# Optimization experiments

Hardware: AMD Instinct MI355X
Metric: run time of the kernel (lower is better)

Reference implementation:

```python
import jax, jax.numpy as jnp
import numpy as np

B, N, C = 8, 4096, 512
NUM_HEADS = 8
HEAD_DIM = C // NUM_HEADS
POS_RES = 32  # only table with res <= max_resolution=32


def _interp_linear(pos, out_len):
    # F.interpolate(mode='linear', align_corners=False) along the length axis (axis 1)
    in_len = pos.shape[1]
    scale = in_len / out_len
    coords = (jnp.arange(out_len, dtype=jnp.float32) + 0.5) * scale - 0.5
    coords = jnp.clip(coords, 0.0, in_len - 1)
    i0 = jnp.floor(coords).astype(jnp.int32)
    i1 = jnp.minimum(i0 + 1, in_len - 1)
    w = (coords - i0.astype(jnp.float32))[None, :, None]
    return pos[:, i0, :] * (1.0 - w) + pos[:, i1, :] * w


def setup_inputs():
    key = jax.random.key(0)
    k = jax.random.split(key, 4)
    x = jax.random.normal(k[0], (B, N, C), jnp.float32)
    pos_32 = jax.random.normal(k[1], (1, POS_RES ** 3, C), jnp.float32)  # torch.randn init
    s = 1.0 / np.sqrt(C)
    w_qkv = jax.random.normal(k[2], (C, 3 * C), jnp.float32) * s
    b_qkv = jnp.zeros((3 * C,), jnp.float32)
    w_proj = jax.random.normal(k[3], (C, C), jnp.float32) * s
    b_proj = jnp.zeros((C,), jnp.float32)
    return {"x": x, "pos_32": pos_32, "w_qkv": w_qkv, "b_qkv": b_qkv,
            "w_proj": w_proj, "b_proj": b_proj, "resolution": 16}


def reference(x, pos_32, w_qkv, b_qkv, w_proj, b_proj, resolution):
    Bx, Nx, Cx = x.shape
    target_len = resolution ** 3  # 4096 -> nearest table pos_32 is interpolated down
    pos = pos_32 if pos_32.shape[1] == target_len else _interp_linear(pos_32, target_len)
    if pos.shape[1] == Nx:
        x = x + pos
    qkv = (x @ w_qkv + b_qkv).reshape(Bx, Nx, 3, NUM_HEADS, HEAD_DIM)
    q, k, v = qkv[:, :, 0], qkv[:, :, 1], qkv[:, :, 2]  # each [B, N, H, D]
    # Faithful to source: q,k,v are NOT permuted to [B,H,N,D], so q @ k.T
    # contracts head_dim per token, yielding [B, N, H, H] head-axis attention.
    attn = jnp.einsum('bnid,bnjd->bnij', q, k) / np.sqrt(HEAD_DIM)
    attn = jax.nn.softmax(attn, axis=-1)
    out = jnp.einsum('bnij,bnjd->bnid', attn, v)  # [B, N, H, D]
    # torch: .transpose(1, 2).reshape(B, N, C) -> flatten of [B, H, N, D]
    out = jnp.transpose(out, (0, 2, 1, 3)).reshape(Bx, Nx, Cx)
    return out @ w_proj + b_proj
```

## Files before the change

kernel.cpp:

```cpp
#include <hip/hip_runtime.h>
#include <hip/hip_bf16.h>

using bf16 = __hip_bfloat16;
typedef __attribute__((ext_vector_type(8))) short short8;
typedef __attribute__((ext_vector_type(4))) float f32x4;

#define AS1U(p) ((const __attribute__((address_space(1))) unsigned int*)(p))
#define AS3U(p) ((__attribute__((address_space(3))) unsigned int*)(p))

__device__ __forceinline__ float bflo(unsigned u) { return __uint_as_float(u << 16); }
__device__ __forceinline__ float bfhi(unsigned u) { return __uint_as_float(u & 0xffff0000u); }
__device__ __forceinline__ unsigned short f2bf(float f) {
    union { float f; unsigned u; } v{f};
    unsigned r = v.u + 0x7fffu + ((v.u >> 16) & 1u);
    return (unsigned short)(r >> 16);
}

__global__ __launch_bounds__(256) void kprep(const float* __restrict__ wq,
                                             const float* __restrict__ wp,
                                             const float* __restrict__ x,
                                             const float* __restrict__ pos,
                                             bf16* __restrict__ wqT,
                                             bf16* __restrict__ wpT,
                                             bf16* __restrict__ xp) {
    int bid = blockIdx.x;
    __shared__ float t[32][33];
    if (bid < 1024) {
        const float* in; bf16* out; int Cc, bx, by;
        if (bid < 768) { in = wq; out = wqT; Cc = 1536; bx = bid % 48; by = bid / 48; }
        else { int i = bid - 768; in = wp; out = wpT; Cc = 512; bx = i & 15; by = i >> 4; }
        const int R = 512;
        int tx = threadIdx.x & 31, ty = threadIdx.x >> 5;
        int c0 = bx * 32, r0 = by * 32;
#pragma unroll
        for (int i = 0; i < 4; ++i)
            t[ty + i * 8][tx] = in[(size_t)(r0 + ty + i * 8) * Cc + c0 + tx];
        __syncthreads();
#pragma unroll
        for (int i = 0; i < 4; ++i)
            out[(size_t)(c0 + ty + i * 8) * R + r0 + tx] = __float2bfloat16(t[tx][ty + i * 8]);
    } else {
        size_t idx4 = (size_t)(bid - 1024) * 256 + threadIdx.x;
        size_t e = idx4 * 4;
        int c = (int)(e & 511);
        size_t m = e >> 9;
        int n = (int)(m & 4095);
        float4 xv = *(const float4*)(x + e);
        float4 p3 = *(const float4*)(pos + (size_t)(n * 8 + 3) * 512 + c);
        float4 p4 = *(const float4*)(pos + (size_t)(n * 8 + 4) * 512 + c);
        unsigned r[2];
        float v0 = xv.x + 0.5f * (p3.x + p4.x);
        float v1 = xv.y + 0.5f * (p3.y + p4.y);
        float v2 = xv.z + 0.5f * (p3.z + p4.z);
        float v3 = xv.w + 0.5f * (p3.w + p4.w);
        r[0] = (unsigned)f2bf(v0) | ((unsigned)f2bf(v1) << 16);
        r[1] = (unsigned)f2bf(v2) | ((unsigned)f2bf(v3) << 16);
        *(uint2*)(xp + e) = *(uint2*)r;
    }
}

template <typename OutT>
__global__ __launch_bounds__(512, 2) void kgemm8(const bf16* __restrict__ A,
                                                 const bf16* __restrict__ Bt,
                                                 const float* __restrict__ bias,
                                                 OutT* __restrict__ C,
                                                 int M, int N, int K_) {
    constexpr int K = 512;
    __shared__ __align__(16) char smem[131072];
    const int tid = threadIdx.x;
    const int lane = tid & 63, wave = tid >> 6;
    const int wm = wave >> 2, wn = wave & 3;
    const int fr = lane & 15;
    const int g = lane >> 4;

    const int p_rd = (((fr & 1) << 2) | g) ^ ((fr >> 1) & 7);
    const int tbA = (wm * 64 + (fr >> 1)) * 128 + p_rd * 16;
    const int tbB = (wn * 32 + (fr >> 1)) * 128 + p_rd * 16;

    const int ntn = N >> 8;
    const int nwg = gridDim.x;
    const int bid = blockIdx.x;
    const int swz = (bid & 7) * (nwg >> 3) + (bid >> 3);
    const int bm = (swz / ntn) << 8;
    const int bn = (swz % ntn) << 8;

    const int q = (lane & 7) ^ (lane >> 3);
    const int srow = wave * 32 + 2 * (lane >> 3) + ((q >> 2) & 1);
    const int scol = (q & 3) * 8;
    const bf16* sA[2]; const bf16* sB[2];
#pragma unroll
    for (int g2 = 0; g2 < 2; ++g2) {
        sA[g2] = A  + (size_t)(bm + srow + g2 * 16) * K + scol;
        sB[g2] = Bt + (size_t)(bn + srow + g2 * 16) * K + scol;
    }
    const int dA0 = wave * 2048, dA1 = wave * 2048 + 1024;

    f32x4 acc[8][4];
#pragma unroll
    for (int i = 0; i < 8; ++i)
#pragma unroll
        for (int j = 0; j < 4; ++j) acc[i][j] = f32x4{0.f, 0.f, 0.f, 0.f};

    auto stageA = [&](int kt, int slot) {
        char* d = smem + slot * 32768;
        __builtin_amdgcn_global_load_lds(AS1U(sA[0] + kt * 32), AS3U(d + dA0), 16, 0, 0);
        __builtin_amdgcn_global_load_lds(AS1U(sA[1] + kt * 32), AS3U(d + dA1), 16, 0, 0);
    };
    auto stageB = [&](int kt, int slot) {
        char* d = smem + slot * 32768 + 16384;
        __builtin_amdgcn_global_load_lds(AS1U(sB[0] + kt * 32), AS3U(d + dA0), 16, 0, 0);
        __builtin_amdgcn_global_load_lds(AS1U(sB[1] + kt * 32), AS3U(d + dA1), 16, 0, 0);
    };

    stageA(0, 0); stageB(0, 0);
    stageA(1, 1); stageB(1, 1);
    stageA(2, 2); stageB(2, 2);
    asm volatile("s_waitcnt vmcnt(8)" ::: "memory");
    __builtin_amdgcn_s_barrier();

#pragma unroll
    for (int t = 0; t < 16; ++t) {
        const int rd = t & 3, wrs = (t + 3) & 3;
        const char* pa = smem + rd * 32768;
        const char* pb = pa + 16384;
        if (t < 13) { stageA(t + 3, wrs); stageB(t + 3, wrs); }
        short8 af[8], bfr[4];
#pragma unroll
        for (int mi = 0; mi < 8; ++mi) af[mi] = *(const short8*)(pa + tbA + mi * 1024);
#pragma unroll
        for (int nj = 0; nj < 4; ++nj) bfr[nj] = *(const short8*)(pb + tbB + nj * 1024);
#pragma unroll
        for (int mi = 0; mi < 8; ++mi)
#pragma unroll
            for (int nj = 0; nj < 4; ++nj)
                acc[mi][nj] = __builtin_amdgcn_mfma_f32_16x16x32_bf16(af[mi], bfr[nj], acc[mi][nj], 0, 0, 0);
        asm volatile("s_waitcnt lgkmcnt(0)" ::: "memory");
        if (t <= 12)      asm volatile("s_waitcnt vmcnt(8)" ::: "memory");
        else if (t == 13) asm volatile("s_waitcnt vmcnt(4)" ::: "memory");
        else if (t == 14) asm volatile("s_waitcnt vmcnt(0)" ::: "memory");
        __builtin_amdgcn_sched_barrier(0);
        __builtin_amdgcn_s_barrier();
    }

#pragma unroll
    for (int mi = 0; mi < 8; ++mi) {
#pragma unroll
        for (int nj = 0; nj < 4; ++nj) {
            int col = bn + wn * 64 + nj * 16 + fr;
            int row0 = bm + wm * 128 + mi * 16 + (lane >> 4) * 4;
            float bv = bias[col];
#pragma unroll
            for (int rr = 0; rr < 4; ++rr) {
                float val = acc[mi][nj][rr] + bv;
                if constexpr (sizeof(OutT) == 2)
                    C[(size_t)(row0 + rr) * N + col] = (OutT)__float2bfloat16(val);
                else
                    C[(size_t)(row0 + rr) * N + col] = (OutT)val;
            }
        }
    }
}

__global__ __launch_bounds__(256) void kattn(const bf16* __restrict__ qkv,
                                             bf16* __restrict__ oscr) {
    int T = blockIdx.x * 256 + threadIdx.x;
    int token = T >> 3, head = T & 7;
    int b = token >> 12, n = token & 4095;
    const bf16* row = qkv + (size_t)token * 1536;

    uint4 qp[8];
#pragma unroll
    for (int c = 0; c < 8; ++c) qp[c] = *(const uint4*)(row + head * 64 + c * 8);

    float s[8];
#pragma unroll
    for (int j = 0; j < 8; ++j) {
        float acc = 0.f;
#pragma unroll
        for (int c = 0; c < 8; ++c) {
            uint4 kp = *(const uint4*)(row + 512 + j * 64 + c * 8);
            const unsigned* ku = &kp.x; const unsigned* qu = &qp[c].x;
#pragma unroll
            for (int w = 0; w < 4; ++w) {
                acc = fmaf(bflo(qu[w]), bflo(ku[w]), acc);
                acc = fmaf(bfhi(qu[w]), bfhi(ku[w]), acc);
            }
        }
        s[j] = acc * 0.125f;
    }
    float mx = s[0];
#pragma unroll
    for (int j = 1; j < 8; ++j) mx = fmaxf(mx, s[j]);
    float sum = 0.f;
#pragma unroll
    for (int j = 0; j < 8; ++j) { s[j] = __expf(s[j] - mx); sum += s[j]; }
    float inv = 1.f / sum;
#pragma unroll
    for (int j = 0; j < 8; ++j) s[j] *= inv;

    float o[64];
#pragma unroll
    for (int d = 0; d < 64; ++d) o[d] = 0.f;
#pragma unroll
    for (int j = 0; j < 8; ++j) {
        float pj = s[j];
#pragma unroll
        for (int c = 0; c < 8; ++c) {
            uint4 vp = *(const uint4*)(row + 1024 + j * 64 + c * 8);
            const unsigned* vu = &vp.x;
#pragma unroll
            for (int w = 0; w < 4; ++w) {
                o[c * 8 + w * 2]     = fmaf(pj, bflo(vu[w]), o[c * 8 + w * 2]);
                o[c * 8 + w * 2 + 1] = fmaf(pj, bfhi(vu[w]), o[c * 8 + w * 2 + 1]);
            }
        }
    }
    size_t orow = (size_t)b * 4096 + head * 512 + (n >> 3);
    bf16* op = oscr + orow * 512 + (n & 7) * 64;
#pragma unroll
    for (int c = 0; c < 8; ++c) {
        unsigned rr[4];
#pragma unroll
        for (int w = 0; w < 4; ++w)
            rr[w] = (unsigned)f2bf(o[c * 8 + w * 2]) | ((unsigned)f2bf(o[c * 8 + w * 2 + 1]) << 16);
        *(uint4*)(op + c * 8) = *(uint4*)rr;
    }
}

extern "C" void kernel_launch(void* const* d_in, const int* in_sizes, int n_in,
                              void* d_out, int out_size, void* d_ws, size_t ws_size,
                              hipStream_t stream) {
    const float* x      = (const float*)d_in[0];
    const float* pos32  = (const float*)d_in[1];
    const float* w_qkv  = (const float*)d_in[2];
    const float* b_qkv  = (const float*)d_in[3];
    const float* w_proj = (const float*)d_in[4];
    const float* b_proj = (const float*)d_in[5];

    char* ws = (char*)d_ws;
    bf16* xp   = (bf16*)(ws);
    bf16* qkv  = (bf16*)(ws + 33554432);
    bf16* wqT  = (bf16*)(ws + 134217728);
    bf16* wpT  = (bf16*)(ws + 135790592);
    bf16* ascr = xp;

    kprep<<<17408, 256, 0, stream>>>(w_qkv, w_proj, x, pos32, wqT, wpT, xp);
    kgemm8<bf16><<<768, 512, 0, stream>>>(xp, wqT, b_qkv, qkv, 32768, 1536, 512);
    kattn<<<1024, 256, 0, stream>>>(qkv, ascr);
    kgemm8<float><<<256, 512, 0, stream>>>(ascr, wpT, b_proj, (float*)d_out, 32768, 512, 512);
}
```

Measured before the change: 143.1 us.

## Fuse positional-embedding add and bf16 cast of x into the QKV GEMM A-load

The prep kernel now only computes a 4096x512 bf16 averaged positional table instead of writing a full B*N*C bf16 copy of x+pos. A new QKV GEMM kernel reads fp32 x directly, adds the bf16 positional row, converts to bf16 in registers and writes the result into LDS, while B is still staged with global_load_lds. This removes a full write and re-read of the activation intermediate. In exchange the GEMM reads twice as many bytes for A (fp32) and does the conversion on its critical path, and the workspace layout is rearranged so posavg shares space with the attention scratch.

```diff
diff --git a/kernel.cpp b/kernel.cpp
--- a/kernel.cpp
+++ b/kernel.cpp
@@ -18,11 +18,10 @@
 
 __global__ __launch_bounds__(256) void kprep(const float* __restrict__ wq,
                                              const float* __restrict__ wp,
-                                             const float* __restrict__ x,
                                              const float* __restrict__ pos,
                                              bf16* __restrict__ wqT,
                                              bf16* __restrict__ wpT,
-                                             bf16* __restrict__ xp) {
+                                             bf16* __restrict__ posavg) {
     int bid = blockIdx.x;
     __shared__ float t[32][33];
     if (bid < 1024) {
@@ -40,22 +39,147 @@
         for (int i = 0; i < 4; ++i)
             out[(size_t)(c0 + ty + i * 8) * R + r0 + tx] = __float2bfloat16(t[tx][ty + i * 8]);
     } else {
-        size_t idx4 = (size_t)(bid - 1024) * 256 + threadIdx.x;
-        size_t e = idx4 * 4;
+        size_t idx = (size_t)(bid - 1024) * 256 + threadIdx.x;
+        size_t e = idx * 8;
+        int n = (int)(e >> 9);
         int c = (int)(e & 511);
-        size_t m = e >> 9;
-        int n = (int)(m & 4095);
-        float4 xv = *(const float4*)(x + e);
-        float4 p3 = *(const float4*)(pos + (size_t)(n * 8 + 3) * 512 + c);
-        float4 p4 = *(const float4*)(pos + (size_t)(n * 8 + 4) * 512 + c);
-        unsigned r[2];
-        float v0 = xv.x + 0.5f * (p3.x + p4.x);
-        float v1 = xv.y + 0.5f * (p3.y + p4.y);
-        float v2 = xv.z + 0.5f * (p3.z + p4.z);
-        float v3 = xv.w + 0.5f * (p3.w + p4.w);
-        r[0] = (unsigned)f2bf(v0) | ((unsigned)f2bf(v1) << 16);
-        r[1] = (unsigned)f2bf(v2) | ((unsigned)f2bf(v3) << 16);
-        *(uint2*)(xp + e) = *(uint2*)r;
+        const float* p3 = pos + (size_t)(n * 8 + 3) * 512 + c;
+        const float* p4 = pos + (size_t)(n * 8 + 4) * 512 + c;
+        unsigned r[4];
+#pragma unroll
+        for (int h = 0; h < 2; ++h) {
+            float4 a = *(const float4*)(p3 + h * 4);
+            float4 b = *(const float4*)(p4 + h * 4);
+            float v0 = 0.5f * (a.x + b.x), v1 = 0.5f * (a.y + b.y);
+            float v2 = 0.5f * (a.z + b.z), v3 = 0.5f * (a.w + b.w);
+            r[h * 2]     = (unsigned)f2bf(v0) | ((unsigned)f2bf(v1) << 16);
+            r[h * 2 + 1] = (unsigned)f2bf(v2) | ((unsigned)f2bf(v3) << 16);
+        }
+        *(uint4*)(posavg + e) = *(uint4*)r;
+    }
+}
+
+
+__global__ __launch_bounds__(512, 2) void kgemmF(const float* __restrict__ X,
+                                                 const bf16* __restrict__ posavg,
+                                                 const bf16* __restrict__ Bt,
+                                                 const float* __restrict__ bias,
+                                                 bf16* __restrict__ C,
+                                                 int M, int N) {
+    constexpr int K = 512;
+    __shared__ __align__(16) char smem[131072];
+    const int tid = threadIdx.x;
+    const int lane = tid & 63, wave = tid >> 6;
+    const int wm = wave >> 2, wn = wave & 3;
+    const int fr = lane & 15;
+    const int g = lane >> 4;
+
+    const int p_rd = (((fr & 1) << 2) | g) ^ ((fr >> 1) & 7);
+    const int tbA = (wm * 64 + (fr >> 1)) * 128 + p_rd * 16;
+    const int tbB = (wn * 32 + (fr >> 1)) * 128 + p_rd * 16;
+
+    const int ntn = N >> 8;
+    const int nwg = gridDim.x;
+    const int bid = blockIdx.x;
+    const int swz = (bid & 7) * (nwg >> 3) + (bid >> 3);
+    const int bm = (swz / ntn) << 8;
+    const int bn = (swz % ntn) << 8;
+
+    const int q = (lane & 7) ^ (lane >> 3);
+    const int srow = wave * 32 + 2 * (lane >> 3) + ((q >> 2) & 1);
+    const int scol = (q & 3) * 8;
+    const bf16* sB[2];
+#pragma unroll
+    for (int g2 = 0; g2 < 2; ++g2)
+        sB[g2] = Bt + (size_t)(bn + srow + g2 * 16) * K + scol;
+    const int dA0 = wave * 2048, dA1 = wave * 2048 + 1024;
+    auto stageB = [&](int kt, int slot) {
+        char* d = smem + slot * 32768 + 16384;
+        __builtin_amdgcn_global_load_lds(AS1U(sB[0] + kt * 32), AS3U(d + dA0), 16, 0, 0);
+        __builtin_amdgcn_global_load_lds(AS1U(sB[1] + kt * 32), AS3U(d + dA1), 16, 0, 0);
+    };
+
+    const int rA = wave * 32 + (lane >> 1);
+    const int gA0 = (lane & 1) * 2;
+    const int mrow = bm + rA;
+    const float* xrow = X + (size_t)mrow * K;
+    const bf16* prow = posavg + (size_t)(mrow & 4095) * K;
+    const int abase = (rA >> 4) * 1024 + ((rA >> 1) & 7) * 128;
+    const int asw = (rA >> 1) & 7, ahi = (rA & 1) << 2;
+    const int ad0 = abase + (((gA0)     | ahi) ^ asw) * 16;
+    const int ad1 = abase + (((gA0 + 1) | ahi) ^ asw) * 16;
+
+    f32x4 ax[4]; uint4 ap[2];
+    auto ldA = [&](int kt) {
+        const float* xs = xrow + kt * 32 + gA0 * 8;
+#pragma unroll
+        for (int i = 0; i < 4; ++i) ax[i] = *(const f32x4*)(xs + i * 4);
+        const bf16* ps = prow + kt * 32 + gA0 * 8;
+        ap[0] = *(const uint4*)(ps);
+        ap[1] = *(const uint4*)(ps + 8);
+    };
+    auto cvtWriteA = [&](int slot) {
+        char* d = smem + slot * 32768;
+#pragma unroll
+        for (int j = 0; j < 2; ++j) {
+            const float* xf = (const float*)&ax[2 * j];
+            const unsigned* pu = &ap[j].x;
+            unsigned out[4];
+#pragma unroll
+            for (int w = 0; w < 4; ++w) {
+                float lo = xf[2 * w]     + bflo(pu[w]);
+                float hi = xf[2 * w + 1] + bfhi(pu[w]);
+                out[w] = (unsigned)f2bf(lo) | ((unsigned)f2bf(hi) << 16);
+            }
+            *(uint4*)(d + (j ? ad1 : ad0)) = *(uint4*)out;
+        }
+    };
+
+    f32x4 acc[8][4];
+#pragma unroll
+    for (int i = 0; i < 8; ++i)
+#pragma unroll
+        for (int j = 0; j < 4; ++j) acc[i][j] = f32x4{0.f, 0.f, 0.f, 0.f};
+
+    stageB(0, 0); stageB(1, 1); stageB(2, 2);
+    ldA(0); cvtWriteA(0);
+    ldA(1); cvtWriteA(1);
+    ldA(2);
+    __syncthreads();
+
+#pragma unroll
+    for (int t = 0; t < 16; ++t) {
+        const int rd = t & 3;
+        const char* pa = smem + rd * 32768;
+        const char* pb = pa + 16384;
+        if (t <= 13) cvtWriteA((t + 2) & 3);
+        if (t < 13) { stageB(t + 3, (t + 3) & 3); ldA(t + 3); }
+        short8 af[8], bfr[4];
+#pragma unroll
+        for (int mi = 0; mi < 8; ++mi) af[mi] = *(const short8*)(pa + tbA + mi * 1024);
+#pragma unroll
+        for (int nj = 0; nj < 4; ++nj) bfr[nj] = *(const short8*)(pb + tbB + nj * 1024);
+#pragma unroll
+        for (int mi = 0; mi < 8; ++mi)
+#pragma unroll
+            for (int nj = 0; nj < 4; ++nj)
+                acc[mi][nj] = __builtin_amdgcn_mfma_f32_16x16x32_bf16(af[mi], bfr[nj], acc[mi][nj], 0, 0, 0);
+        asm volatile("s_waitcnt lgkmcnt(0)" ::: "memory");
+        __builtin_amdgcn_sched_barrier(0);
+        __builtin_amdgcn_s_barrier();
+    }
+
+#pragma unroll
+    for (int mi = 0; mi < 8; ++mi) {
+#pragma unroll
+        for (int nj = 0; nj < 4; ++nj) {
+            int col = bn + wn * 64 + nj * 16 + fr;
+            int row0 = bm + wm * 128 + mi * 16 + (lane >> 4) * 4;
+            float bv = bias[col];
+#pragma unroll
+            for (int rr = 0; rr < 4; ++rr)
+                C[(size_t)(row0 + rr) * N + col] = (bf16)__float2bfloat16(acc[mi][nj][rr] + bv);
+        }
     }
 }
 
@@ -238,14 +362,14 @@
     const float* b_proj = (const float*)d_in[5];
 
     char* ws = (char*)d_ws;
-    bf16* xp   = (bf16*)(ws);
-    bf16* qkv  = (bf16*)(ws + 33554432);
-    bf16* wqT  = (bf16*)(ws + 134217728);
-    bf16* wpT  = (bf16*)(ws + 135790592);
-    bf16* ascr = xp;
-
-    kprep<<<17408, 256, 0, stream>>>(w_qkv, w_proj, x, pos32, wqT, wpT, xp);
-    kgemm8<bf16><<<768, 512, 0, stream>>>(xp, wqT, b_qkv, qkv, 32768, 1536, 512);
+    bf16* qkv    = (bf16*)(ws);
+    bf16* ascr   = (bf16*)(ws + 100663296);
+    bf16* posavg = (bf16*)(ws + 100663296);
+    bf16* wqT    = (bf16*)(ws + 134217728);
+    bf16* wpT    = (bf16*)(ws + 135790592);
+
+    kprep<<<2048, 256, 0, stream>>>(w_qkv, w_proj, pos32, wqT, wpT, posavg);
+    kgemmF<<<768, 512, 0, stream>>>(x, posavg, wqT, b_qkv, qkv, 32768, 1536);
     kattn<<<1024, 256, 0, stream>>>(qkv, ascr);
     kgemm8<float><<<256, 512, 0, stream>>>(ascr, wpT, b_proj, (float*)d_out, 32768, 512, 512);
 }
```

Result: slower. 189.0 us (+32.1%).

## Use persistent QKV GEMM looping over three N tiles with cross-tile prefetch

Applied to the files above, without the earlier changes.

Replaces the 768-block QKV GEMM with a 256-block kernel where each block handles one 256-row M tile and iterates over three 256-column N tiles. The K-loop pipeline continues across N tiles, so the next tile's first stages are prefetched during the tail of the current one. This is meant to remove pipeline fill/drain bubbles and per-block launch overhead. The cost is fewer blocks (256 on a large-CU GPU), which may leave the device underfilled, and the A tile is re-streamed for each N tile rather than reused.

```diff
diff --git a/kernel.cpp b/kernel.cpp
--- a/kernel.cpp
+++ b/kernel.cpp
@@ -59,6 +59,106 @@
     }
 }
 
+
+__global__ __launch_bounds__(512, 2) void kgemmP(const bf16* __restrict__ A,
+                                                 const bf16* __restrict__ Bt,
+                                                 const float* __restrict__ bias,
+                                                 bf16* __restrict__ C) {
+    constexpr int K = 512, N = 1536;
+    __shared__ __align__(16) char smem[131072];
+    const int tid = threadIdx.x;
+    const int lane = tid & 63, wave = tid >> 6;
+    const int wm = wave >> 2, wn = wave & 3;
+    const int fr = lane & 15;
+    const int g = lane >> 4;
+
+    const int p_rd = (((fr & 1) << 2) | g) ^ ((fr >> 1) & 7);
+    const int tbA = (wm * 64 + (fr >> 1)) * 128 + p_rd * 16;
+    const int tbB = (wn * 32 + (fr >> 1)) * 128 + p_rd * 16;
+
+    const int bid = blockIdx.x;
+    const int bm = (bid & 127) << 8;
+    const int bngrp = bid >> 7;
+
+    const int q = (lane & 7) ^ (lane >> 3);
+    const int srow = wave * 32 + 2 * (lane >> 3) + ((q >> 2) & 1);
+    const int scol = (q & 3) * 8;
+    const bf16* sA0 = A + (size_t)(bm + srow) * K + scol;
+    const bf16* sA1 = A + (size_t)(bm + srow + 16) * K + scol;
+    const bf16* b00 = Bt + (size_t)(bngrp * 768 +   0 + srow) * K + scol;
+    const bf16* b01 = Bt + (size_t)(bngrp * 768 +  16 + srow) * K + scol;
+    const bf16* b10 = b00 + (size_t)256 * K;
+    const bf16* b11 = b01 + (size_t)256 * K;
+    const bf16* b20 = b00 + (size_t)512 * K;
+    const bf16* b21 = b01 + (size_t)512 * K;
+    const int dA0 = wave * 2048, dA1 = wave * 2048 + 1024;
+
+    auto stageA = [&](int kt, int slot) {
+        char* d = smem + slot * 32768;
+        __builtin_amdgcn_global_load_lds(AS1U(sA0 + kt * 32), AS3U(d + dA0), 16, 0, 0);
+        __builtin_amdgcn_global_load_lds(AS1U(sA1 + kt * 32), AS3U(d + dA1), 16, 0, 0);
+    };
+    auto stageBp = [&](const bf16* p0, const bf16* p1, int kt, int slot) {
+        char* d = smem + slot * 32768 + 16384;
+        __builtin_amdgcn_global_load_lds(AS1U(p0 + kt * 32), AS3U(d + dA0), 16, 0, 0);
+        __builtin_amdgcn_global_load_lds(AS1U(p1 + kt * 32), AS3U(d + dA1), 16, 0, 0);
+    };
+
+    f32x4 acc[8][4];
+
+    stageA(0, 0); stageBp(b00, b01, 0, 0);
+    stageA(1, 1); stageBp(b00, b01, 1, 1);
+    stageA(2, 2); stageBp(b00, b01, 2, 2);
+    asm volatile("s_waitcnt vmcnt(8)" ::: "memory");
+    __builtin_amdgcn_s_barrier();
+
+    const bf16 *curB0 = b00, *curB1 = b01, *nxtB0 = b10, *nxtB1 = b11;
+    for (int j = 0; j < 3; ++j) {
+#pragma unroll
+        for (int i = 0; i < 8; ++i)
+#pragma unroll
+            for (int jj = 0; jj < 4; ++jj) acc[i][jj] = f32x4{0.f, 0.f, 0.f, 0.f};
+#pragma unroll
+        for (int t = 0; t < 16; ++t) {
+            const int rd = t & 3, wrs = (t + 3) & 3;
+            const char* pa = smem + rd * 32768;
+            const char* pb = pa + 16384;
+            if (t <= 12) { stageA(t + 3, wrs); stageBp(curB0, curB1, t + 3, wrs); }
+            else if (j < 2) { stageA(t - 13, wrs); stageBp(nxtB0, nxtB1, t - 13, wrs); }
+            short8 af[8], bfr[4];
+#pragma unroll
+            for (int mi = 0; mi < 8; ++mi) af[mi] = *(const short8*)(pa + tbA + mi * 1024);
+#pragma unroll
+            for (int nj = 0; nj < 4; ++nj) bfr[nj] = *(const short8*)(pb + tbB + nj * 1024);
+#pragma unroll
+            for (int mi = 0; mi < 8; ++mi)
+#pragma unroll
+                for (int nj = 0; nj < 4; ++nj)
+                    acc[mi][nj] = __builtin_amdgcn_mfma_f32_16x16x32_bf16(af[mi], bfr[nj], acc[mi][nj], 0, 0, 0);
+            asm volatile("s_waitcnt lgkmcnt(0)" ::: "memory");
+            if (j < 2 || t <= 12)  asm volatile("s_waitcnt vmcnt(8)" ::: "memory");
+            else if (t == 13)      asm volatile("s_waitcnt vmcnt(4)" ::: "memory");
+            else if (t == 14)      asm volatile("s_waitcnt vmcnt(0)" ::: "memory");
+            __builtin_amdgcn_sched_barrier(0);
+            __builtin_amdgcn_s_barrier();
+        }
+        const int bn = bngrp * 768 + j * 256;
+#pragma unroll
+        for (int mi = 0; mi < 8; ++mi) {
+#pragma unroll
+            for (int nj = 0; nj < 4; ++nj) {
+                int col = bn + wn * 64 + nj * 16 + fr;
+                int row0 = bm + wm * 128 + mi * 16 + (lane >> 4) * 4;
+                float bv = bias[col];
+#pragma unroll
+                for (int rr = 0; rr < 4; ++rr)
+                    C[(size_t)(row0 + rr) * N + col] = (bf16)__float2bfloat16(acc[mi][nj][rr] + bv);
+            }
+        }
+        curB0 = nxtB0; curB1 = nxtB1; nxtB0 = b20; nxtB1 = b21;
+    }
+}
+
 template <typename OutT>
 __global__ __launch_bounds__(512, 2) void kgemm8(const bf16* __restrict__ A,
                                                  const bf16* __restrict__ Bt,
@@ -245,7 +345,7 @@
     bf16* ascr = xp;
 
     kprep<<<17408, 256, 0, stream>>>(w_qkv, w_proj, x, pos32, wqT, wpT, xp);
-    kgemm8<bf16><<<768, 512, 0, stream>>>(xp, wqT, b_qkv, qkv, 32768, 1536, 512);
+    kgemmP<<<256, 512, 0, stream>>>(xp, wqT, b_qkv, qkv);
     kattn<<<1024, 256, 0, stream>>>(qkv, ascr);
     kgemm8<float><<<256, 512, 0, stream>>>(ascr, wpT, b_proj, (float*)d_out, 32768, 512, 512);
 }
```

Measured after the change: 159.9 us. +11.8%, slower.

## Replace 256x256 GEMM with 128x128 double-buffered tile kernel; widen prep vectors

Applied to the files above, without the earlier changes.

The GEMM kernel drops from 256x256 tiles with 512 threads and a 4-stage LDS ring to 128x128 tiles with 256 threads and a 2-stage double buffer synchronized by __syncthreads. This gives more workgroups (3072 and 1024 instead of 768 and 256) for better CU occupancy and tail balance, at the cost of less data reuse per tile and a shallower prefetch pipeline. The prep kernel now handles 8 elements per thread with 16-byte stores, halving its grid size.

```diff
diff --git a/kernel.cpp b/kernel.cpp
--- a/kernel.cpp
+++ b/kernel.cpp
@@ -40,114 +40,106 @@
         for (int i = 0; i < 4; ++i)
             out[(size_t)(c0 + ty + i * 8) * R + r0 + tx] = __float2bfloat16(t[tx][ty + i * 8]);
     } else {
-        size_t idx4 = (size_t)(bid - 1024) * 256 + threadIdx.x;
-        size_t e = idx4 * 4;
+        size_t idx8 = (size_t)(bid - 1024) * 256 + threadIdx.x;
+        size_t e = idx8 * 8;
         int c = (int)(e & 511);
-        size_t m = e >> 9;
-        int n = (int)(m & 4095);
-        float4 xv = *(const float4*)(x + e);
-        float4 p3 = *(const float4*)(pos + (size_t)(n * 8 + 3) * 512 + c);
-        float4 p4 = *(const float4*)(pos + (size_t)(n * 8 + 4) * 512 + c);
-        unsigned r[2];
-        float v0 = xv.x + 0.5f * (p3.x + p4.x);
-        float v1 = xv.y + 0.5f * (p3.y + p4.y);
-        float v2 = xv.z + 0.5f * (p3.z + p4.z);
-        float v3 = xv.w + 0.5f * (p3.w + p4.w);
-        r[0] = (unsigned)f2bf(v0) | ((unsigned)f2bf(v1) << 16);
-        r[1] = (unsigned)f2bf(v2) | ((unsigned)f2bf(v3) << 16);
-        *(uint2*)(xp + e) = *(uint2*)r;
-    }
-}
+        int n = (int)((e >> 9) & 4095);
+        const float* xs = x + e;
+        const float* p3 = pos + (size_t)(n * 8 + 3) * 512 + c;
+        const float* p4 = pos + (size_t)(n * 8 + 4) * 512 + c;
+        unsigned r[4];
+#pragma unroll
+        for (int h = 0; h < 2; ++h) {
+            float4 xv = *(const float4*)(xs + h * 4);
+            float4 a = *(const float4*)(p3 + h * 4);
+            float4 b = *(const float4*)(p4 + h * 4);
+            float v0 = xv.x + 0.5f * (a.x + b.x);
+            float v1 = xv.y + 0.5f * (a.y + b.y);
+            float v2 = xv.z + 0.5f * (a.z + b.z);
+            float v3 = xv.w + 0.5f * (a.w + b.w);
+            r[h * 2]     = (unsigned)f2bf(v0) | ((unsigned)f2bf(v1) << 16);
+            r[h * 2 + 1] = (unsigned)f2bf(v2) | ((unsigned)f2bf(v3) << 16);
+        }
+        *(uint4*)(xp + e) = *(uint4*)r;
+    }
+}
+
 
 template <typename OutT>
-__global__ __launch_bounds__(512, 2) void kgemm8(const bf16* __restrict__ A,
-                                                 const bf16* __restrict__ Bt,
-                                                 const float* __restrict__ bias,
-                                                 OutT* __restrict__ C,
-                                                 int M, int N, int K_) {
+__global__ __launch_bounds__(256) void kgemm4(const bf16* __restrict__ A,
+                                              const bf16* __restrict__ Bt,
+                                              const float* __restrict__ bias,
+                                              OutT* __restrict__ C,
+                                              int N) {
     constexpr int K = 512;
-    __shared__ __align__(16) char smem[131072];
+    __shared__ __align__(16) char smem[32768];
     const int tid = threadIdx.x;
     const int lane = tid & 63, wave = tid >> 6;
-    const int wm = wave >> 2, wn = wave & 3;
+    const int wm = wave >> 1, wn = wave & 1;
     const int fr = lane & 15;
     const int g = lane >> 4;
 
-    const int p_rd = (((fr & 1) << 2) | g) ^ ((fr >> 1) & 7);
-    const int tbA = (wm * 64 + (fr >> 1)) * 128 + p_rd * 16;
-    const int tbB = (wn * 32 + (fr >> 1)) * 128 + p_rd * 16;
-
-    const int ntn = N >> 8;
+    const int p_rd = (g | ((fr & 1) << 2)) ^ ((fr >> 1) & 7);
+    const int tbA = wm * 4096 + ((fr >> 1) & 7) * 128 + p_rd * 16;
+    const int tbB = wn * 4096 + ((fr >> 1) & 7) * 128 + p_rd * 16;
+
+    const int ntn = N >> 7;
     const int nwg = gridDim.x;
     const int bid = blockIdx.x;
     const int swz = (bid & 7) * (nwg >> 3) + (bid >> 3);
-    const int bm = (swz / ntn) << 8;
-    const int bn = (swz % ntn) << 8;
-
-    const int q = (lane & 7) ^ (lane >> 3);
-    const int srow = wave * 32 + 2 * (lane >> 3) + ((q >> 2) & 1);
-    const int scol = (q & 3) * 8;
-    const bf16* sA[2]; const bf16* sB[2];
-#pragma unroll
-    for (int g2 = 0; g2 < 2; ++g2) {
-        sA[g2] = A  + (size_t)(bm + srow + g2 * 16) * K + scol;
-        sB[g2] = Bt + (size_t)(bn + srow + g2 * 16) * K + scol;
-    }
-    const int dA0 = wave * 2048, dA1 = wave * 2048 + 1024;
-
-    f32x4 acc[8][4];
-#pragma unroll
-    for (int i = 0; i < 8; ++i)
+    const int bm = (swz / ntn) << 7;
+    const int bn = (swz % ntn) << 7;
+
+    const int q0 = (tid & 7) ^ ((tid >> 3) & 7);
+    const int r0 = ((tid >> 6) << 4) + (((tid >> 3) & 7) << 1) + (q0 >> 2);
+    const int o0 = (q0 & 3) * 8;
+    const bf16* sA0 = A  + (size_t)(bm + r0) * K + o0;
+    const bf16* sA1 = A  + (size_t)(bm + r0 + 64) * K + o0;
+    const bf16* sB0 = Bt + (size_t)(bn + r0) * K + o0;
+    const bf16* sB1 = Bt + (size_t)(bn + r0 + 64) * K + o0;
+    const int d0 = tid * 16;
+
+    f32x4 acc[4][4];
+#pragma unroll
+    for (int i = 0; i < 4; ++i)
 #pragma unroll
         for (int j = 0; j < 4; ++j) acc[i][j] = f32x4{0.f, 0.f, 0.f, 0.f};
 
-    auto stageA = [&](int kt, int slot) {
-        char* d = smem + slot * 32768;
-        __builtin_amdgcn_global_load_lds(AS1U(sA[0] + kt * 32), AS3U(d + dA0), 16, 0, 0);
-        __builtin_amdgcn_global_load_lds(AS1U(sA[1] + kt * 32), AS3U(d + dA1), 16, 0, 0);
+    auto stage = [&](int kt, int slot) {
+        char* d = smem + slot * 16384;
+        __builtin_amdgcn_global_load_lds(AS1U(sA0 + kt * 32), AS3U(d + d0), 16, 0, 0);
+        __builtin_amdgcn_global_load_lds(AS1U(sA1 + kt * 32), AS3U(d + 4096 + d0), 16, 0, 0);
+        __builtin_amdgcn_global_load_lds(AS1U(sB0 + kt * 32), AS3U(d + 8192 + d0), 16, 0, 0);
+        __builtin_amdgcn_global_load_lds(AS1U(sB1 + kt * 32), AS3U(d + 12288 + d0), 16, 0, 0);
     };
-    auto stageB = [&](int kt, int slot) {
-        char* d = smem + slot * 32768 + 16384;
-        __builtin_amdgcn_global_load_lds(AS1U(sB[0] + kt * 32), AS3U(d + dA0), 16, 0, 0);
-        __builtin_amdgcn_global_load_lds(AS1U(sB[1] + kt * 32), AS3U(d + dA1), 16, 0, 0);
-    };
-
-    stageA(0, 0); stageB(0, 0);
-    stageA(1, 1); stageB(1, 1);
-    stageA(2, 2); stageB(2, 2);
-    asm volatile("s_waitcnt vmcnt(8)" ::: "memory");
-    __builtin_amdgcn_s_barrier();
+
+    stage(0, 0);
+    __syncthreads();
 
 #pragma unroll
     for (int t = 0; t < 16; ++t) {
-        const int rd = t & 3, wrs = (t + 3) & 3;
-        const char* pa = smem + rd * 32768;
-        const char* pb = pa + 16384;
-        if (t < 13) { stageA(t + 3, wrs); stageB(t + 3, wrs); }
-        short8 af[8], bfr[4];
-#pragma unroll
-        for (int mi = 0; mi < 8; ++mi) af[mi] = *(const short8*)(pa + tbA + mi * 1024);
+        const char* pa = smem + (t & 1) * 16384;
+        const char* pb = pa + 8192;
+        if (t < 15) stage(t + 1, (t + 1) & 1);
+        short8 af[4], bfr[4];
+#pragma unroll
+        for (int mi = 0; mi < 4; ++mi) af[mi] = *(const short8*)(pa + tbA + mi * 1024);
 #pragma unroll
         for (int nj = 0; nj < 4; ++nj) bfr[nj] = *(const short8*)(pb + tbB + nj * 1024);
 #pragma unroll
-        for (int mi = 0; mi < 8; ++mi)
+        for (int mi = 0; mi < 4; ++mi)
 #pragma unroll
             for (int nj = 0; nj < 4; ++nj)
                 acc[mi][nj] = __builtin_amdgcn_mfma_f32_16x16x32_bf16(af[mi], bfr[nj], acc[mi][nj], 0, 0, 0);
-        asm volatile("s_waitcnt lgkmcnt(0)" ::: "memory");
-        if (t <= 12)      asm volatile("s_waitcnt vmcnt(8)" ::: "memory");
-        else if (t == 13) asm volatile("s_waitcnt vmcnt(4)" ::: "memory");
-        else if (t == 14) asm volatile("s_waitcnt vmcnt(0)" ::: "memory");
-        __builtin_amdgcn_sched_barrier(0);
-        __builtin_amdgcn_s_barrier();
-    }
-
-#pragma unroll
-    for (int mi = 0; mi < 8; ++mi) {
+        __syncthreads();
+    }
+
+#pragma unroll
+    for (int mi = 0; mi < 4; ++mi) {
 #pragma unroll
         for (int nj = 0; nj < 4; ++nj) {
             int col = bn + wn * 64 + nj * 16 + fr;
-            int row0 = bm + wm * 128 + mi * 16 + (lane >> 4) * 4;
+            int row0 = bm + wm * 64 + mi * 16 + (lane >> 4) * 4;
             float bv = bias[col];
 #pragma unroll
             for (int rr = 0; rr < 4; ++rr) {
@@ -244,8 +236,8 @@
     bf16* wpT  = (bf16*)(ws + 135790592);
     bf16* ascr = xp;
 
-    kprep<<<17408, 256, 0, stream>>>(w_qkv, w_proj, x, pos32, wqT, wpT, xp);
-    kgemm8<bf16><<<768, 512, 0, stream>>>(xp, wqT, b_qkv, qkv, 32768, 1536, 512);
+    kprep<<<9216, 256, 0, stream>>>(w_qkv, w_proj, x, pos32, wqT, wpT, xp);
+    kgemm4<bf16><<<3072, 256, 0, stream>>>(xp, wqT, b_qkv, qkv, 1536);
     kattn<<<1024, 256, 0, stream>>>(qkv, ascr);
-    kgemm8<float><<<256, 512, 0, stream>>>(ascr, wpT, b_proj, (float*)d_out, 32768, 512, 512);
-}
+    kgemm4<float><<<1024, 256, 0, stream>>>(ascr, wpT, b_proj, (float*)d_out, 512);
+}
```

Measured after the change: 155.0 us. 1.08x slower.
